# Kernel tuning notes

Hardware: AMD Instinct MI355X
Metric: run time of the kernel (lower is better)

Reference implementation:

```python
import jax, jax.numpy as jnp
import numpy as np

WS = 7        # window size
IMG = 56      # input resolution (H = W)
BATCH = 32    # image batch
DIM = 384
HEADS = 12
HEAD_DIM = DIM // HEADS
N = WS * WS                      # tokens per window = 49
NW = (IMG // WS) * (IMG // WS)   # windows per image = 64
B_ = BATCH * NW                  # 2048
TBL = (2 * WS - 1) ** 2          # 169


def _rel_index(ws):
    # standard Swin relative position index, values in [0, (2ws-1)^2)
    coords = np.stack(np.meshgrid(np.arange(ws), np.arange(ws), indexing='ij'))
    coords = coords.reshape(2, -1)                       # (2, N)
    rel = coords[:, :, None] - coords[:, None, :]        # (2, N, N)
    rel = rel.transpose(1, 2, 0).astype(np.int64).copy()
    rel[:, :, 0] += ws - 1
    rel[:, :, 1] += ws - 1
    rel[:, :, 0] *= 2 * ws - 1
    return rel.sum(-1)                                   # (N, N)


def _shift_mask(H, W, ws, shift):
    # shifted-window attention mask, (nW, N, N) with 0 / -100
    img = np.zeros((H, W))
    cnt = 0
    for hs in (slice(0, -ws), slice(-ws, -shift), slice(-shift, None)):
        for wsl in (slice(0, -ws), slice(-ws, -shift), slice(-shift, None)):
            img[hs, wsl] = cnt
            cnt += 1
    win = img.reshape(H // ws, ws, W // ws, ws).transpose(0, 2, 1, 3).reshape(-1, ws * ws)
    diff = win[:, None, :] - win[:, :, None]
    return np.where(diff != 0, -100.0, 0.0).astype(np.float32)


def setup_inputs() -> dict:
    key = jax.random.key(0)
    ks = jax.random.split(key, 7)
    s = 0.02
    return {
        'x': jax.random.normal(ks[0], (B_, N, DIM), jnp.float32),
        'mask': jnp.asarray(_shift_mask(IMG, IMG, WS, WS // 2)),
        'rpe_indices': jnp.asarray(_rel_index(WS)),
        'qkv_w': jax.random.normal(ks[1], (3 * DIM, DIM), jnp.float32) * s,
        'qkv_b': jnp.zeros((3 * DIM,), jnp.float32),
        'proj_w': jax.random.normal(ks[2], (DIM, DIM), jnp.float32) * s,
        'proj_b': jnp.zeros((DIM,), jnp.float32),
        'q_rpe': jax.random.normal(ks[3], (HEADS, HEAD_DIM, TBL), jnp.float32) * s,
        'k_rpe': jax.random.normal(ks[4], (HEADS, HEAD_DIM, TBL), jnp.float32) * s,
        'v_rpe': jax.random.normal(ks[5], (HEADS, TBL, HEAD_DIM), jnp.float32) * s,
    }


def reference(x, mask, rpe_indices, qkv_w, qkv_b, proj_w, proj_b, q_rpe, k_rpe, v_rpe):
    B, n, C = x.shape
    h, hd = q_rpe.shape[0], q_rpe.shape[1]
    scale = hd ** -0.5

    qkv = x @ qkv_w.T + qkv_b                                   # (B, N, 3C)
    qkv = qkv.reshape(B, n, 3, h, hd).transpose(2, 0, 3, 1, 4)   # (3, B, h, N, hd)
    q, k, v = qkv[0] * scale, qkv[1], qkv[2]

    attn = jnp.einsum('bhid,bhjd->bhij', q, k)                   # (B, h, N, N)

    # Contextual q/k bias. The torch code does b_q.flatten(2)[:, :, rpe_indices]
    # with rpe_indices in [0, TBL): gathering from the flattened (N*TBL) axis with
    # indices < TBL selects row 0 of the N axis, i.e. b_q[:, :, 0, rpe_indices].
    # We compute only that row, which is mathematically identical.
    bq0 = jnp.einsum('bhd,hdt->bht', q[:, :, 0], q_rpe)          # (B, h, TBL)
    bk0 = jnp.einsum('bhd,hdt->bht', k[:, :, 0], k_rpe)          # (B, h, TBL)
    attn = attn + (bq0 + bk0)[:, :, rpe_indices]                 # gather -> (B, h, N, N)

    nW = mask.shape[0]
    attn = attn.reshape(B // nW, nW, h, n, n) + mask[None, :, None]
    attn = jax.nn.softmax(attn.reshape(B, h, n, n), axis=-1)

    # contextual v bias: w = v_rpe[:, rpe_indices] -> (h, N, N, hd)
    w = v_rpe[:, rpe_indices.reshape(-1)].reshape(h, n, n, hd)
    r_v = jnp.einsum('bhij,hijd->bihd', attn, w).reshape(B, n, C)

    out = jnp.einsum('bhij,bhjd->bihd', attn, v).reshape(B, n, C) + r_v
    out = out @ proj_w.T + proj_b
    return out, attn
```

## Files before the change

kernel.cpp:

```cpp
#include <hip/hip_runtime.h>


typedef unsigned int u32;
typedef unsigned short u16;
typedef __attribute__((ext_vector_type(8))) short bf16x8;
typedef __attribute__((ext_vector_type(4))) float f32x4;

#define SCALE 0.17677669529663687f

__device__ __forceinline__ u16 f2b(float f) {
  union { float f; u32 u; } c; c.f = f;
  u32 u = c.u;
  return (u16)((u + 0x7FFFu + ((u >> 16) & 1u)) >> 16);
}
__device__ __forceinline__ float b2f(u16 s) {
  union { float f; u32 u; } c; c.u = ((u32)s) << 16;
  return c.f;
}
__device__ __forceinline__ void async16(void* lds, const void* g) {
  __builtin_amdgcn_global_load_lds(
      (const __attribute__((address_space(1))) u32*)g,
      (__attribute__((address_space(3))) u32*)lds, 16, 0, 0);
}

__global__ __launch_bounds__(256) void k_cast(const float* __restrict__ s,
                                              u16* __restrict__ d, int n4) {
  int i = blockIdx.x * 256 + threadIdx.x;
  int str = gridDim.x * 256;
  for (; i < n4; i += str) {
    float4 v = ((const float4*)s)[i];
    ushort4 o;
    o.x = f2b(v.x); o.y = f2b(v.y); o.z = f2b(v.z); o.w = f2b(v.w);
    ((ushort4*)d)[i] = o;
  }
}

__global__ __launch_bounds__(256) void k_mbi(const float* __restrict__ mask,
                                             const int* __restrict__ idx,
                                             u16* __restrict__ mbi) {
  int i = blockIdx.x * 256 + threadIdx.x;
  if (i >= 64 * 2401) return;
  int p = i % 2401;
  mbi[i] = (u16)(idx[p] | ((mask[i] != 0.0f) ? 256 : 0));
}

__global__ __launch_bounds__(256) void k_qkv(
    const u16* __restrict__ A, const u16* __restrict__ Bw,
    const float* __restrict__ bias, u16* __restrict__ outq) {
  int bx0 = blockIdx.x;
  int bx = (bx0 & 7) * 882 + (bx0 >> 3);
  int mt = bx / 9, nt = bx - mt * 9;
  size_t m0 = (size_t)mt * 128;
  int n0 = nt * 128;
  int tid = threadIdx.x;
  int w = tid >> 6, l = tid & 63;
  int wm = w >> 1, wn = w & 1;
  int lr = l & 15, lg = l >> 4, lk8 = lg << 3;
  __shared__ u16 At[128 * 32];
  __shared__ u16 Bt[128 * 32];
  f32x4 acc[4][4] = {};
  int row = tid >> 2, c8 = (tid & 3) << 3;
  const u16* gA = A + (m0 + row) * 384 + c8;
  const u16* gA2 = A + (m0 + row + 64) * 384 + c8;
  const u16* gB = Bw + (size_t)(n0 + row) * 384 + c8;
  const u16* gB2 = Bw + (size_t)(n0 + row + 64) * 384 + c8;
  for (int ks = 0; ks < 12; ++ks) {
    int k0 = ks * 32;
    async16(At + tid * 8, gA + k0);
    async16(At + (256 + tid) * 8, gA2 + k0);
    async16(Bt + tid * 8, gB + k0);
    async16(Bt + (256 + tid) * 8, gB2 + k0);
    __syncthreads();
    bf16x8 af[4], bfr[4];
#pragma unroll
    for (int mi = 0; mi < 4; ++mi)
      af[mi] = *(const bf16x8*)&At[(wm * 64 + mi * 16 + lr) * 32 + lk8];
#pragma unroll
    for (int ni = 0; ni < 4; ++ni)
      bfr[ni] = *(const bf16x8*)&Bt[(wn * 64 + ni * 16 + lr) * 32 + lk8];
#pragma unroll
    for (int mi = 0; mi < 4; ++mi)
#pragma unroll
      for (int ni = 0; ni < 4; ++ni)
        acc[mi][ni] = __builtin_amdgcn_mfma_f32_16x16x32_bf16(af[mi], bfr[ni], acc[mi][ni], 0, 0, 0);
    __syncthreads();
  }
#pragma unroll
  for (int ni = 0; ni < 4; ++ni) {
    int cc = n0 + wn * 64 + ni * 16 + lr;
    float bv = bias[cc];
    float sc = (cc < 384) ? SCALE : 1.0f;
#pragma unroll
    for (int mi = 0; mi < 4; ++mi)
#pragma unroll
      for (int r = 0; r < 4; ++r) {
        size_t rr = m0 + wm * 64 + mi * 16 + lg * 4 + r;
        outq[rr * 1152 + cc] = f2b((acc[mi][ni][r] + bv) * sc);
      }
  }
}

__global__ __launch_bounds__(256) void k_bqk(
    const u16* __restrict__ qkv, const float* __restrict__ q_rpe,
    const float* __restrict__ k_rpe, float* __restrict__ bqk) {
  int bx = blockIdx.x;
  int mtile = bx / 12, h = bx % 12;
  int b0 = mtile * 64;
  int tid = threadIdx.x;
  int w = tid >> 6, l = tid & 63;
  int lr = l & 15, g = l >> 4;

  __shared__ __align__(16) u16 At[64 * 64];
  __shared__ __align__(16) u16 Bt[192 * 64];

  {
    int m = tid >> 2;
#pragma unroll
    for (int rnd = 0; rnd < 2; ++rnd) {
      int c = (tid & 3) + rnd * 4;
      const u16* src = qkv + (size_t)(b0 + m) * 56448 + h * 32 +
                       ((c < 4) ? c * 8 : 384 + (c - 4) * 8);
      bf16x8 v = *(const bf16x8*)src;
      int byte = (m * 128 + c * 16) ^ ((m & 7) << 4);
      *(bf16x8*)((char*)At + byte) = v;
    }
  }
  if (tid < 192) {
    int t = tid;
#pragma unroll
    for (int c = 0; c < 8; ++c) {
      u16 pk[8];
#pragma unroll
      for (int e = 0; e < 8; ++e) {
        int d = (c & 3) * 8 + e;
        float v = 0.f;
        if (t < 169)
          v = (c < 4) ? q_rpe[(h * 32 + d) * 169 + t]
                      : k_rpe[(h * 32 + d) * 169 + t];
        pk[e] = f2b(v);
      }
      int byte = (t * 128 + c * 16) ^ ((t & 7) << 4);
      *(bf16x8*)((char*)Bt + byte) = *(bf16x8*)pk;
    }
  }
  __syncthreads();

  f32x4 acc[12] = {};
  bf16x8 af[2];
#pragma unroll
  for (int ks = 0; ks < 2; ++ks) {
    int row = w * 16 + lr;
    af[ks] = *(const bf16x8*)((const char*)At +
              ((row * 128 + ks * 64 + g * 16) ^ ((row & 7) << 4)));
  }
#pragma unroll
  for (int nt = 0; nt < 12; ++nt) {
#pragma unroll
    for (int ks = 0; ks < 2; ++ks) {
      int t = nt * 16 + lr;
      bf16x8 bf = *(const bf16x8*)((const char*)Bt +
                   ((t * 128 + ks * 64 + g * 16) ^ ((t & 7) << 4)));
      acc[nt] = __builtin_amdgcn_mfma_f32_16x16x32_bf16(af[ks], bf, acc[nt], 0, 0, 0);
    }
  }
#pragma unroll
  for (int nt = 0; nt < 12; ++nt) {
    int t = nt * 16 + lr;
    if (t < 169) {
#pragma unroll
      for (int r = 0; r < 4; ++r) {
        int b = b0 + w * 16 + g * 4 + r;
        bqk[((size_t)b * 12 + h) * 169 + t] = acc[nt][r];
      }
    }
  }
}

__global__ __launch_bounds__(256) void k_attn(
    const u16* __restrict__ qkv, const float* __restrict__ bqkG,
    const u16* __restrict__ mbi,
    float* __restrict__ attn, u16* __restrict__ attnB, u16* __restrict__ o1) {
  int blk0 = blockIdx.x;
  int blk = (blk0 & 7) * 768 + (blk0 >> 3);
  int b = blk / 3, hg = blk % 3;
  int tid = threadIdx.x, w = tid >> 6, l = tid & 63;
  int h = hg * 4 + w;
  int lr = l & 15, g = l >> 4;

  __shared__ __align__(16) char R[32704];
  __shared__ __align__(16) u16 vL[4][2048];
  u16* mbiL = (u16*)R;
  float* bqkL = (float*)(R + 4832);
  u16* pL = (u16*)(R + 7600);
  float* aS = (float*)R;

  const u16* qbase = qkv + (size_t)b * 49 * 1152 + h * 32;
  const u16* kbase = qbase + 384;
  const u16* vbase = qbase + 768;

  {
    const u16* mrow = mbi + (size_t)(b & 63) * 2401;
    for (int p = tid; p < 2401; p += 256) mbiL[p] = mrow[p];
  }
  u16* vw = &vL[w][0];
#pragma unroll
  for (int p = 0; p < 4; ++p) {
    int j = p * 16 + (l >> 2);
    int jr = (j < 49) ? j : 48;
    async16(vw + p * 512 + l * 8, vbase + (size_t)jr * 1152 + (l & 3) * 8);
  }
  {
    const float* bg = bqkG + ((size_t)b * 12 + h) * 169;
#pragma unroll
    for (int t0 = 0; t0 < 192; t0 += 64) {
      int t = t0 + l;
      if (t < 169) bqkL[w * 172 + t] = bg[t];
    }
  }

  bf16x8 qf[4], kf[4];
#pragma unroll
  for (int t = 0; t < 4; ++t) {
    int qi = t * 16 + lr;
    int qir = (qi < 49) ? qi : 48;
    qf[t] = *(const bf16x8*)(qbase + (size_t)qir * 1152 + g * 8);
    kf[t] = *(const bf16x8*)(kbase + (size_t)qir * 1152 + g * 8);
  }

  f32x4 S[4][4] = {};
#pragma unroll
  for (int mt = 0; mt < 4; ++mt)
#pragma unroll
    for (int nt = 0; nt < 4; ++nt)
      S[mt][nt] = __builtin_amdgcn_mfma_f32_16x16x32_bf16(kf[mt], qf[nt], S[mt][nt], 0, 0, 0);

  __syncthreads();

#pragma unroll
  for (int nt = 0; nt < 4; ++nt) {
    int qi = nt * 16 + lr;
#pragma unroll
    for (int mt = 0; mt < 4; ++mt)
#pragma unroll
      for (int r = 0; r < 4; ++r) {
        int kj = mt * 16 + g * 4 + r;
        float s = S[mt][nt][r];
        if (qi < 49 && kj < 49) {
          u16 t = mbiL[qi * 49 + kj];
          s += bqkL[w * 172 + (t & 255)] - 100.f * (float)(t >> 8);
        } else {
          s = -1e9f;
        }
        S[mt][nt][r] = s;
      }
  }

  float rinv[4];
#pragma unroll
  for (int nt = 0; nt < 4; ++nt) {
    float m = -1e30f;
#pragma unroll
    for (int mt = 0; mt < 4; ++mt)
#pragma unroll
      for (int r = 0; r < 4; ++r) m = fmaxf(m, S[mt][nt][r]);
    m = fmaxf(m, __shfl_xor(m, 16, 64));
    m = fmaxf(m, __shfl_xor(m, 32, 64));
    float sum = 0.f;
#pragma unroll
    for (int mt = 0; mt < 4; ++mt)
#pragma unroll
      for (int r = 0; r < 4; ++r) {
        float e = __expf(S[mt][nt][r] - m);
        S[mt][nt][r] = e;
        sum += e;
      }
    sum += __shfl_xor(sum, 16, 64);
    sum += __shfl_xor(sum, 32, 64);
    rinv[nt] = 1.f / sum;
  }

  {
    u16* abase = attnB + ((size_t)(b * 12 + h) * 49) * 64;
#pragma unroll
    for (int nt = 0; nt < 4; ++nt) {
      int qi = nt * 16 + lr;
      if (qi < 49) {
        float riv = rinv[nt];
#pragma unroll
        for (int mt = 0; mt < 4; ++mt) {
          u32 w0 = (u32)f2b(S[mt][nt][0] * riv) | ((u32)f2b(S[mt][nt][1] * riv) << 16);
          u32 w1 = (u32)f2b(S[mt][nt][2] * riv) | ((u32)f2b(S[mt][nt][3] * riv) << 16);
          uint2 pk = {w0, w1};
          *(uint2*)(abase + (size_t)qi * 64 + mt * 16 + g * 4) = pk;
        }
      }
    }
  }

  u16* pw = pL + w * 3136;
#pragma unroll
  for (int nt = 0; nt < 4; ++nt) {
    int qi = nt * 16 + lr;
    if (qi < 49) {
      int swz = (qi & 7) << 4;
#pragma unroll
      for (int mt = 0; mt < 4; ++mt) {
        u32 w0 = (u32)f2b(S[mt][nt][0]) | ((u32)f2b(S[mt][nt][1]) << 16);
        u32 w1 = (u32)f2b(S[mt][nt][2]) | ((u32)f2b(S[mt][nt][3]) << 16);
        int off = (qi * 128 + mt * 32 + g * 8) ^ swz;
        uint2 pk = {w0, w1};
        *(uint2*)((char*)pw + off) = pk;
      }
    }
  }

  f32x4 O[2][4] = {};
#pragma unroll
  for (int ks = 0; ks < 2; ++ks) {
    bf16x8 pb[4];
#pragma unroll
    for (int nti = 0; nti < 4; ++nti) {
      int qi = nti * 16 + lr;
      int qir = (qi < 49) ? qi : 48;
      int off = (qir * 128 + ks * 64 + g * 16) ^ ((qir & 7) << 4);
      pb[nti] = *(const bf16x8*)((const char*)pw + off);
    }
    bf16x8 va[2];
#pragma unroll
    for (int mtd = 0; mtd < 2; ++mtd)
#pragma unroll
      for (int jj = 0; jj < 8; ++jj)
        va[mtd][jj] = (short)vw[(ks * 32 + g * 8 + jj) * 32 + mtd * 16 + lr];
#pragma unroll
    for (int mtd = 0; mtd < 2; ++mtd)
#pragma unroll
      for (int nti = 0; nti < 4; ++nti)
        O[mtd][nti] = __builtin_amdgcn_mfma_f32_16x16x32_bf16(va[mtd], pb[nti], O[mtd][nti], 0, 0, 0);
  }

  {
    u16* ob = o1 + (size_t)b * 49 * 384 + h * 32;
#pragma unroll
    for (int nti = 0; nti < 4; ++nti) {
      int i = nti * 16 + lr;
      if (i < 49) {
        float riv = rinv[nti];
#pragma unroll
        for (int mtd = 0; mtd < 2; ++mtd) {
          u32 w0 = (u32)f2b(O[mtd][nti][0] * riv) | ((u32)f2b(O[mtd][nti][1] * riv) << 16);
          u32 w1 = (u32)f2b(O[mtd][nti][2] * riv) | ((u32)f2b(O[mtd][nti][3] * riv) << 16);
          uint2 pk = {w0, w1};
          *(uint2*)&ob[(size_t)i * 384 + mtd * 16 + g * 4] = pk;
        }
      }
    }
  }

  __syncthreads();
  float* aw = aS + w * 1216;
  float* ao = attn + (size_t)(b * 12 + h) * 2401;
#pragma unroll
  for (int half = 0; half < 2; ++half) {
    int lo = half * 1204;
#pragma unroll
    for (int nt = 0; nt < 4; ++nt) {
      int qi = nt * 16 + lr;
      if (qi < 49) {
        float riv = rinv[nt];
#pragma unroll
        for (int mt = 0; mt < 4; ++mt)
#pragma unroll
          for (int r = 0; r < 4; ++r) {
            int kj = mt * 16 + g * 4 + r;
            if (kj < 49) {
              int p = qi * 49 + kj - lo;
              if (p >= 0 && p < 1204) aw[p] = S[mt][nt][r] * riv;
            }
          }
      }
    }
    asm volatile("s_waitcnt lgkmcnt(0)" ::: "memory");
    int lim = half ? 1197 : 1204;
#pragma unroll
    for (int it = 0; it < 19; ++it) {
      int p = l + it * 64;
      if (p < lim) ao[lo + p] = aw[p];
    }
    asm volatile("s_waitcnt lgkmcnt(0)" ::: "memory");
  }
}

__global__ __launch_bounds__(256) void k_rv(
    const u16* __restrict__ attnB, const int* __restrict__ idx,
    const float* __restrict__ v_rpe, u16* __restrict__ o1) {
  int bx = blockIdx.x;
  int bc = bx & 7;
  int hi = bx >> 3;
  int i = hi % 49, h = hi / 49;
  int b0 = bc * 256;
  int tid = threadIdx.x;
  int w = tid >> 6, l = tid & 63;
  int lr = l & 15, g = l >> 4;

  __shared__ __align__(16) u16 wT[32 * 64];

  if (tid < 196) {
    int j = tid >> 2, d0 = (tid & 3) * 8;
    const float* vr = v_rpe + ((size_t)h * 169 + idx[i * 49 + j]) * 32 + d0;
    float4 a = *(const float4*)vr;
    float4 bvv = *(const float4*)(vr + 4);
    float el[8] = {a.x, a.y, a.z, a.w, bvv.x, bvv.y, bvv.z, bvv.w};
#pragma unroll
    for (int e = 0; e < 8; ++e) {
      int d = d0 + e;
      int byte = (d * 128 + j * 2) ^ ((d & 7) << 4);
      *(u16*)((char*)wT + byte) = f2b(el[e]);
    }
  } else {
    int t = tid - 196;
    int j = 49 + (t >> 2), d0 = (t & 3) * 8;
#pragma unroll
    for (int e = 0; e < 8; ++e) {
      int d = d0 + e;
      int byte = (d * 128 + j * 2) ^ ((d & 7) << 4);
      *(u16*)((char*)wT + byte) = 0;
    }
  }
  __syncthreads();

  f32x4 acc[2][4] = {};
#pragma unroll
  for (int ks = 0; ks < 2; ++ks) {
    bf16x8 af[2], bfr[4];
#pragma unroll
    for (int mt = 0; mt < 2; ++mt) {
      int d = mt * 16 + lr;
      int byte = (d * 128 + ks * 64 + g * 16) ^ ((d & 7) << 4);
      af[mt] = *(const bf16x8*)((const char*)wT + byte);
    }
#pragma unroll
    for (int nt = 0; nt < 4; ++nt) {
      int row = w * 64 + nt * 16 + lr;
      const u16* ar = attnB + (((size_t)(b0 + row) * 12 + h) * 49 + i) * 64;
      bfr[nt] = *(const bf16x8*)(ar + ks * 32 + g * 8);
    }
#pragma unroll
    for (int mt = 0; mt < 2; ++mt)
#pragma unroll
      for (int nt = 0; nt < 4; ++nt)
        acc[mt][nt] = __builtin_amdgcn_mfma_f32_16x16x32_bf16(af[mt], bfr[nt], acc[mt][nt], 0, 0, 0);
  }

#pragma unroll
  for (int nt = 0; nt < 4; ++nt) {
    int bl = w * 64 + nt * 16 + lr;
    u16* ob = o1 + ((size_t)(b0 + bl) * 49 + i) * 384 + h * 32;
#pragma unroll
    for (int mt = 0; mt < 2; ++mt) {
      int d = mt * 16 + g * 4;
      uint2 old = *(uint2*)&ob[d];
      uint2 nw;
      nw.x = (u32)f2b(b2f((u16)(old.x & 0xffff)) + acc[mt][nt][0]) |
             ((u32)f2b(b2f((u16)(old.x >> 16)) + acc[mt][nt][1]) << 16);
      nw.y = (u32)f2b(b2f((u16)(old.y & 0xffff)) + acc[mt][nt][2]) |
             ((u32)f2b(b2f((u16)(old.y >> 16)) + acc[mt][nt][3]) << 16);
      *(uint2*)&ob[d] = nw;
    }
  }
}

__global__ __launch_bounds__(256) void k_proj(
    const u16* __restrict__ A, const u16* __restrict__ Bw,
    const float* __restrict__ bias, float* __restrict__ out) {
  int bx0 = blockIdx.x;
  int bx = (bx0 & 7) * 294 + (bx0 >> 3);
  int mt = bx / 3, nt = bx - mt * 3;
  size_t m0 = (size_t)mt * 128;
  int n0 = nt * 128;
  int tid = threadIdx.x;
  int w = tid >> 6, l = tid & 63;
  int wm = w >> 1, wn = w & 1;
  int lr = l & 15, lg = l >> 4, lk8 = lg << 3;
  __shared__ u16 At[128 * 32];
  __shared__ u16 Bt[128 * 32];
  f32x4 acc[4][4] = {};
  int row = tid >> 2, c8 = (tid & 3) << 3;
  const u16* gA = A + (m0 + row) * 384 + c8;
  const u16* gA2 = A + (m0 + row + 64) * 384 + c8;
  const u16* gB = Bw + (size_t)(n0 + row) * 384 + c8;
  const u16* gB2 = Bw + (size_t)(n0 + row + 64) * 384 + c8;
  for (int ks = 0; ks < 12; ++ks) {
    int k0 = ks * 32;
    async16(At + tid * 8, gA + k0);
    async16(At + (256 + tid) * 8, gA2 + k0);
    async16(Bt + tid * 8, gB + k0);
    async16(Bt + (256 + tid) * 8, gB2 + k0);
    __syncthreads();
    bf16x8 af[4], bfr[4];
#pragma unroll
    for (int mi = 0; mi < 4; ++mi)
      af[mi] = *(const bf16x8*)&At[(wm * 64 + mi * 16 + lr) * 32 + lk8];
#pragma unroll
    for (int ni = 0; ni < 4; ++ni)
      bfr[ni] = *(const bf16x8*)&Bt[(wn * 64 + ni * 16 + lr) * 32 + lk8];
#pragma unroll
    for (int mi = 0; mi < 4; ++mi)
#pragma unroll
      for (int ni = 0; ni < 4; ++ni)
        acc[mi][ni] = __builtin_amdgcn_mfma_f32_16x16x32_bf16(af[mi], bfr[ni], acc[mi][ni], 0, 0, 0);
    __syncthreads();
  }
#pragma unroll
  for (int mi = 0; mi < 4; ++mi)
#pragma unroll
    for (int ni = 0; ni < 4; ++ni)
#pragma unroll
      for (int r = 0; r < 4; ++r) {
        int rr = wm * 64 + mi * 16 + lg * 4 + r;
        int cc = wn * 64 + ni * 16 + lr;
        out[(m0 + rr) * 384 + (size_t)(n0 + cc)] = acc[mi][ni][r] + bias[n0 + cc];
      }
}

extern "C" void kernel_launch(void* const* d_in, const int* in_sizes, int n_in,
                              void* d_out, int out_size, void* d_ws, size_t ws_size,
                              hipStream_t stream) {
  const float* x      = (const float*)d_in[0];
  const float* mask   = (const float*)d_in[1];
  const int*   rpe    = (const int*)d_in[2];
  const float* qkv_w  = (const float*)d_in[3];
  const float* qkv_b  = (const float*)d_in[4];
  const float* proj_w = (const float*)d_in[5];
  const float* proj_b = (const float*)d_in[6];
  const float* q_rpe  = (const float*)d_in[7];
  const float* k_rpe  = (const float*)d_in[8];
  const float* v_rpe  = (const float*)d_in[9];

  float* out   = (float*)d_out;
  float* attn  = out + (size_t)100352 * 384;
  u16*   attnB = (u16*)d_out;

  char* ws = (char*)d_ws;
  u16*   qkvb   = (u16*)ws;
  u16*   wqkvb  = (u16*)(ws + 231211008);
  u16*   wprojb = (u16*)(ws + 232095744);
  u16*   mbi    = (u16*)(ws + 232390656);
  float* bqkG   = (float*)(ws + 232697984);
  u16*   xb     = (u16*)(ws + 249311360);
  u16*   o1     = xb;

  k_cast<<<2048, 256, 0, stream>>>(x, xb, 9633792);
  k_cast<<<432, 256, 0, stream>>>(qkv_w, wqkvb, 110592);
  k_cast<<<144, 256, 0, stream>>>(proj_w, wprojb, 36864);
  k_mbi<<<601, 256, 0, stream>>>(mask, rpe, mbi);
  k_qkv<<<7056, 256, 0, stream>>>(xb, wqkvb, qkv_b, qkvb);
  k_bqk<<<384, 256, 0, stream>>>(qkvb, q_rpe, k_rpe, bqkG);
  k_attn<<<6144, 256, 0, stream>>>(qkvb, bqkG, mbi, attn, attnB, o1);
  k_rv<<<4704, 256, 0, stream>>>(attnB, rpe, v_rpe, o1);
  k_proj<<<2352, 256, 0, stream>>>(o1, wprojb, proj_b, out);
}
```

Baseline: 602.2 us.

## Drop bf16 attention copy; k_rv reads fp32 attn output directly, shrink LDS

Removes the separate bf16 attention-probability buffer that k_attn wrote for k_rv. k_rv now reads the fp32 attn output with unaligned vector loads and converts to bf16 in registers, zeroing padded columns. k_attn gets a smaller per-wave LDS region reused for V, the P slab and the attn staging, with P·V done per 16-row tile and the block barrier removed. This cuts a global write and LDS use, possibly raising occupancy, but k_rv now reads twice the bytes with misaligned loads.

```diff
diff --git a/kernel.cpp b/kernel.cpp
--- a/kernel.cpp
+++ b/kernel.cpp
@@ -5,6 +5,7 @@
 typedef unsigned short u16;
 typedef __attribute__((ext_vector_type(8))) short bf16x8;
 typedef __attribute__((ext_vector_type(4))) float f32x4;
+typedef float f4a __attribute__((ext_vector_type(4), aligned(4)));
 
 #define SCALE 0.17677669529663687f
 
@@ -179,7 +180,7 @@
 __global__ __launch_bounds__(256) void k_attn(
     const u16* __restrict__ qkv, const float* __restrict__ bqkG,
     const u16* __restrict__ mbi,
-    float* __restrict__ attn, u16* __restrict__ attnB, u16* __restrict__ o1) {
+    float* __restrict__ attn, u16* __restrict__ o1) {
   int blk0 = blockIdx.x;
   int blk = (blk0 & 7) * 768 + (blk0 >> 3);
   int b = blk / 3, hg = blk % 3;
@@ -187,12 +188,13 @@
   int h = hg * 4 + w;
   int lr = l & 15, g = l >> 4;
 
-  __shared__ __align__(16) char R[32704];
-  __shared__ __align__(16) u16 vL[4][2048];
-  u16* mbiL = (u16*)R;
-  float* bqkL = (float*)(R + 4832);
-  u16* pL = (u16*)(R + 7600);
-  float* aS = (float*)R;
+  __shared__ __align__(16) char LDSR[32160];
+  u16* mbiL = (u16*)LDSR;
+  float* bqkL = (float*)(LDSR + 4832);
+  char* Uw = LDSR + 7584 + w * 6144;
+  u16* vw = (u16*)Uw;
+  char* slab = Uw + 4096;
+  float* aw = (float*)Uw;
 
   const u16* qbase = qkv + (size_t)b * 49 * 1152 + h * 32;
   const u16* kbase = qbase + 384;
@@ -202,7 +204,6 @@
     const u16* mrow = mbi + (size_t)(b & 63) * 2401;
     for (int p = tid; p < 2401; p += 256) mbiL[p] = mrow[p];
   }
-  u16* vw = &vL[w][0];
 #pragma unroll
   for (int p = 0; p < 4; ++p) {
     int j = p * 16 + (l >> 2);
@@ -279,63 +280,34 @@
     rinv[nt] = 1.f / sum;
   }
 
-  {
-    u16* abase = attnB + ((size_t)(b * 12 + h) * 49) * 64;
-#pragma unroll
-    for (int nt = 0; nt < 4; ++nt) {
-      int qi = nt * 16 + lr;
-      if (qi < 49) {
-        float riv = rinv[nt];
-#pragma unroll
-        for (int mt = 0; mt < 4; ++mt) {
-          u32 w0 = (u32)f2b(S[mt][nt][0] * riv) | ((u32)f2b(S[mt][nt][1] * riv) << 16);
-          u32 w1 = (u32)f2b(S[mt][nt][2] * riv) | ((u32)f2b(S[mt][nt][3] * riv) << 16);
-          uint2 pk = {w0, w1};
-          *(uint2*)(abase + (size_t)qi * 64 + mt * 16 + g * 4) = pk;
-        }
-      }
-    }
-  }
-
-  u16* pw = pL + w * 3136;
+  bf16x8 va[2][2];
+#pragma unroll
+  for (int ks = 0; ks < 2; ++ks)
+#pragma unroll
+    for (int mtd = 0; mtd < 2; ++mtd)
+#pragma unroll
+      for (int jj = 0; jj < 8; ++jj)
+        va[ks][mtd][jj] = (short)vw[(ks * 32 + g * 8 + jj) * 32 + mtd * 16 + lr];
+
+  f32x4 O[2][4] = {};
+  int swz = (lr & 7) << 4;
 #pragma unroll
   for (int nt = 0; nt < 4; ++nt) {
-    int qi = nt * 16 + lr;
-    if (qi < 49) {
-      int swz = (qi & 7) << 4;
-#pragma unroll
-      for (int mt = 0; mt < 4; ++mt) {
-        u32 w0 = (u32)f2b(S[mt][nt][0]) | ((u32)f2b(S[mt][nt][1]) << 16);
-        u32 w1 = (u32)f2b(S[mt][nt][2]) | ((u32)f2b(S[mt][nt][3]) << 16);
-        int off = (qi * 128 + mt * 32 + g * 8) ^ swz;
-        uint2 pk = {w0, w1};
-        *(uint2*)((char*)pw + off) = pk;
-      }
-    }
-  }
-
-  f32x4 O[2][4] = {};
-#pragma unroll
-  for (int ks = 0; ks < 2; ++ks) {
-    bf16x8 pb[4];
-#pragma unroll
-    for (int nti = 0; nti < 4; ++nti) {
-      int qi = nti * 16 + lr;
-      int qir = (qi < 49) ? qi : 48;
-      int off = (qir * 128 + ks * 64 + g * 16) ^ ((qir & 7) << 4);
-      pb[nti] = *(const bf16x8*)((const char*)pw + off);
-    }
-    bf16x8 va[2];
-#pragma unroll
-    for (int mtd = 0; mtd < 2; ++mtd)
-#pragma unroll
-      for (int jj = 0; jj < 8; ++jj)
-        va[mtd][jj] = (short)vw[(ks * 32 + g * 8 + jj) * 32 + mtd * 16 + lr];
-#pragma unroll
-    for (int mtd = 0; mtd < 2; ++mtd)
-#pragma unroll
-      for (int nti = 0; nti < 4; ++nti)
-        O[mtd][nti] = __builtin_amdgcn_mfma_f32_16x16x32_bf16(va[mtd], pb[nti], O[mtd][nti], 0, 0, 0);
+#pragma unroll
+    for (int mt = 0; mt < 4; ++mt) {
+      u32 w0 = (u32)f2b(S[mt][nt][0]) | ((u32)f2b(S[mt][nt][1]) << 16);
+      u32 w1 = (u32)f2b(S[mt][nt][2]) | ((u32)f2b(S[mt][nt][3]) << 16);
+      int off = (lr * 128 + mt * 32 + g * 8) ^ swz;
+      uint2 pk = {w0, w1};
+      *(uint2*)(slab + off) = pk;
+    }
+    bf16x8 pb0 = *(const bf16x8*)(slab + ((lr * 128 + g * 16) ^ swz));
+    bf16x8 pb1 = *(const bf16x8*)(slab + ((lr * 128 + 64 + g * 16) ^ swz));
+#pragma unroll
+    for (int mtd = 0; mtd < 2; ++mtd) {
+      O[mtd][nt] = __builtin_amdgcn_mfma_f32_16x16x32_bf16(va[0][mtd], pb0, O[mtd][nt], 0, 0, 0);
+      O[mtd][nt] = __builtin_amdgcn_mfma_f32_16x16x32_bf16(va[1][mtd], pb1, O[mtd][nt], 0, 0, 0);
+    }
   }
 
   {
@@ -356,42 +328,32 @@
     }
   }
 
-  __syncthreads();
-  float* aw = aS + w * 1216;
   float* ao = attn + (size_t)(b * 12 + h) * 2401;
 #pragma unroll
-  for (int half = 0; half < 2; ++half) {
-    int lo = half * 1204;
-#pragma unroll
-    for (int nt = 0; nt < 4; ++nt) {
-      int qi = nt * 16 + lr;
-      if (qi < 49) {
-        float riv = rinv[nt];
-#pragma unroll
-        for (int mt = 0; mt < 4; ++mt)
-#pragma unroll
-          for (int r = 0; r < 4; ++r) {
-            int kj = mt * 16 + g * 4 + r;
-            if (kj < 49) {
-              int p = qi * 49 + kj - lo;
-              if (p >= 0 && p < 1204) aw[p] = S[mt][nt][r] * riv;
-            }
-          }
-      }
+  for (int nt = 0; nt < 4; ++nt) {
+    int qi = nt * 16 + lr;
+    if (qi < 49) {
+      float riv = rinv[nt];
+#pragma unroll
+      for (int mt = 0; mt < 4; ++mt)
+#pragma unroll
+        for (int r = 0; r < 4; ++r) {
+          int kj = mt * 16 + g * 4 + r;
+          if (kj < 49) aw[lr * 49 + kj] = S[mt][nt][r] * riv;
+        }
     }
     asm volatile("s_waitcnt lgkmcnt(0)" ::: "memory");
-    int lim = half ? 1197 : 1204;
-#pragma unroll
-    for (int it = 0; it < 19; ++it) {
+    int lim = (nt < 3) ? 784 : 49;
+#pragma unroll
+    for (int it = 0; it < 13; ++it) {
       int p = l + it * 64;
-      if (p < lim) ao[lo + p] = aw[p];
-    }
-    asm volatile("s_waitcnt lgkmcnt(0)" ::: "memory");
+      if (p < lim) ao[nt * 784 + p] = aw[p];
+    }
   }
 }
 
 __global__ __launch_bounds__(256) void k_rv(
-    const u16* __restrict__ attnB, const int* __restrict__ idx,
+    const float* __restrict__ attn, const int* __restrict__ idx,
     const float* __restrict__ v_rpe, u16* __restrict__ o1) {
   int bx = blockIdx.x;
   int bc = bx & 7;
@@ -431,24 +393,32 @@
   f32x4 acc[2][4] = {};
 #pragma unroll
   for (int ks = 0; ks < 2; ++ks) {
-    bf16x8 af[2], bfr[4];
+    bf16x8 af[2];
 #pragma unroll
     for (int mt = 0; mt < 2; ++mt) {
       int d = mt * 16 + lr;
       int byte = (d * 128 + ks * 64 + g * 16) ^ ((d & 7) << 4);
       af[mt] = *(const bf16x8*)((const char*)wT + byte);
     }
+    int j0 = ks * 32 + g * 8;
 #pragma unroll
     for (int nt = 0; nt < 4; ++nt) {
-      int row = w * 64 + nt * 16 + lr;
-      const u16* ar = attnB + (((size_t)(b0 + row) * 12 + h) * 49 + i) * 64;
-      bfr[nt] = *(const bf16x8*)(ar + ks * 32 + g * 8);
-    }
-#pragma unroll
-    for (int mt = 0; mt < 2; ++mt)
-#pragma unroll
-      for (int nt = 0; nt < 4; ++nt)
-        acc[mt][nt] = __builtin_amdgcn_mfma_f32_16x16x32_bf16(af[mt], bfr[nt], acc[mt][nt], 0, 0, 0);
+      int bl = w * 64 + nt * 16 + lr;
+      const float* ar = attn + ((size_t)(b0 + bl) * 12 + h) * 2401 +
+                        (size_t)i * 49 + j0;
+      f4a v0 = *(const f4a*)ar;
+      f4a v1 = *(const f4a*)(ar + 4);
+      u16 pk[8];
+#pragma unroll
+      for (int e = 0; e < 8; ++e) {
+        float vv = (e < 4) ? v0[e] : v1[e - 4];
+        pk[e] = (j0 + e < 49) ? f2b(vv) : (u16)0;
+      }
+      bf16x8 bfr = *(bf16x8*)pk;
+#pragma unroll
+      for (int mt = 0; mt < 2; ++mt)
+        acc[mt][nt] = __builtin_amdgcn_mfma_f32_16x16x32_bf16(af[mt], bfr, acc[mt][nt], 0, 0, 0);
+    }
   }
 
 #pragma unroll
@@ -536,9 +506,8 @@
   const float* k_rpe  = (const float*)d_in[8];
   const float* v_rpe  = (const float*)d_in[9];
 
-  float* out   = (float*)d_out;
-  float* attn  = out + (size_t)100352 * 384;
-  u16*   attnB = (u16*)d_out;
+  float* out  = (float*)d_out;
+  float* attn = out + (size_t)100352 * 384;
 
   char* ws = (char*)d_ws;
   u16*   qkvb   = (u16*)ws;
@@ -555,7 +524,7 @@
   k_mbi<<<601, 256, 0, stream>>>(mask, rpe, mbi);
   k_qkv<<<7056, 256, 0, stream>>>(xb, wqkvb, qkv_b, qkvb);
   k_bqk<<<384, 256, 0, stream>>>(qkvb, q_rpe, k_rpe, bqkG);
-  k_attn<<<6144, 256, 0, stream>>>(qkvb, bqkG, mbi, attn, attnB, o1);
-  k_rv<<<4704, 256, 0, stream>>>(attnB, rpe, v_rpe, o1);
+  k_attn<<<6144, 256, 0, stream>>>(qkvb, bqkG, mbi, attn, o1);
+  k_rv<<<4704, 256, 0, stream>>>(attn, rpe, v_rpe, o1);
   k_proj<<<2352, 256, 0, stream>>>(o1, wprojb, proj_b, out);
 }
```

Result: faster. 583.7 us (-3.1%).
